# Kernel tuning notes

Hardware: AMD Instinct MI355X
Metric: run time of the kernel (lower is better)

The kernel has to match this reference:

```python
import jax, jax.numpy as jnp
import numpy as np


def setup_inputs() -> dict:
    key = jax.random.key(0)
    ks = jax.random.split(key, 16)
    B, P, N, E = 16, 12, 20000, 320000
    f32 = jnp.float32
    x = jax.random.normal(ks[0], (B, P, N), f32)
    input_mask = (jax.random.uniform(ks[1], (B, P, N)) > 0.2).astype(f32)  # GAIN observed mask
    noise = jax.random.uniform(ks[2], (B, P, N), f32) * 0.01  # Uniform(0, 0.01) noise matrix
    edge_index = jax.random.randint(ks[3], (2, E), 0, N)
    edge_weights = jax.random.uniform(ks[4], (E,), f32)

    def lin(k, fi, fo):
        return jax.random.normal(k, (fi, fo), f32) * (1.0 / np.sqrt(fi))

    params = dict(
        Wz=lin(ks[5], 2, P), bz=jnp.zeros((P,), f32),
        Wr=lin(ks[6], 2, P), br=jnp.zeros((P,), f32),
        Wh=lin(ks[7], 2, P), bh=jnp.zeros((P,), f32),
        Lz_w=lin(ks[8], 2 * P, P), Lz_b=jnp.zeros((P,), f32),
        Lr_w=lin(ks[9], 2 * P, P), Lr_b=jnp.zeros((P,), f32),
        Lh_w=lin(ks[10], 2 * P, P), Lh_b=jnp.zeros((P,), f32),
        attention=jax.random.uniform(ks[11], (P,), f32),
        W1=lin(ks[12], P, P), b1=jnp.zeros((P,), f32),
        W2=lin(ks[13], P, P), b2=jnp.zeros((P,), f32),
    )
    return dict(x=x, input_mask=input_mask, noise=noise,
                edge_index=edge_index, edge_weights=edge_weights, **params)


def reference(x, input_mask, noise, edge_index, edge_weights,
              Wz, bz, Wr, br, Wh, bh,
              Lz_w, Lz_b, Lr_w, Lr_b, Lh_w, Lh_b,
              attention, W1, b1, W2, b2):
    B, P, N = x.shape
    # GAIN: fill missing entries with small uniform noise
    x = input_mask * x + (1.0 - input_mask) * noise
    # stack([x, mask]) -> [2,B,P,N]; permute(1,3,0,2) -> [B,N,2,P]; we scan over periods
    X = jnp.transpose(jnp.stack([x, input_mask], axis=2), (1, 0, 3, 2))  # [P, B, N, 2]

    # GCNConv symmetric normalization with self-loops (fill_value = 1)
    src, dst = edge_index[0], edge_index[1]
    loop = jnp.arange(N)
    src_sl = jnp.concatenate([src, loop])
    dst_sl = jnp.concatenate([dst, loop])
    w_sl = jnp.concatenate([edge_weights, jnp.ones((N,), x.dtype)])
    deg = jnp.zeros((N,), x.dtype).at[dst_sl].add(w_sl)
    dinv = jnp.where(deg > 0, deg ** -0.5, 0.0)
    norm = dinv[src_sl] * w_sl * dinv[dst_sl]  # [E + N]

    probs = jax.nn.softmax(attention)  # attention over periods
    H0 = jnp.zeros((B, N, P), x.dtype)  # A3TGCN2 never updates H -> each period sees H = 0

    def step(acc, inp):
        Xt, p = inp  # Xt: [B, N, 2]
        # aggregate raw 2-dim features then apply the (linear) GCN weight: same math,
        # far cheaper than gathering the projected [B, E, P] messages
        msgs = Xt[:, src_sl, :] * norm[None, :, None]          # [B, E+N, 2]
        agg = jnp.zeros_like(Xt).at[:, dst_sl, :].add(msgs)    # [B, N, 2]
        xz = agg @ Wz + bz
        xr = agg @ Wr + br
        xh = agg @ Wh + bh
        Z = jax.nn.sigmoid(jnp.concatenate([xz, H0], axis=-1) @ Lz_w + Lz_b)
        R = jax.nn.sigmoid(jnp.concatenate([xr, H0], axis=-1) @ Lr_w + Lr_b)
        Ht = jnp.tanh(jnp.concatenate([xh, H0 * R], axis=-1) @ Lh_w + Lh_b)
        H = Z * H0 + (1.0 - Z) * Ht
        return acc + p * H, None

    H_accum, _ = jax.lax.scan(step, H0, (X, probs))  # [B, N, P]

    # MLP head: ReLU -> Linear -> ReLU -> Linear -> Sigmoid
    h = jax.nn.relu(H_accum)
    h = jax.nn.relu(h @ W1 + b1)
    imput = jax.nn.sigmoid(h @ W2 + b2)               # [B, N, P]
    imputation = jnp.transpose(imput, (0, 2, 1))      # [B, P, N]
    res = input_mask * x + (1.0 - input_mask) * imputation
    return res, imputation
```

## Files before the change

### kernel.cpp

```cpp
#include <hip/hip_runtime.h>

#define NN 20000
#define NE 320000
#define BB 16
#define PP 12
#define NCOL 384
#define OUT_OFF (BB*PP*NN)
#define SLICES 8
#define SCOLS 48

__device__ __forceinline__ float sigmoidf_(float v) {
    return __fdividef(1.f, 1.f + __expf(-v));
}
__device__ __forceinline__ float tanh_fast(float v) {
    v = fminf(fmaxf(v, -15.f), 15.f);
    float e = __expf(-2.f * v);
    return __fdividef(1.f - e, 1.f + e);
}

__global__ __launch_bounds__(256) void init_kernel(float* deg, int* cnt) {
    int i = blockIdx.x * 256 + threadIdx.x;
    if (i < NN) { deg[i] = 1.0f; cnt[i] = 0; }
}

__global__ __launch_bounds__(256) void degcnt_kernel(const int* __restrict__ ei,
                                                     const float* __restrict__ ew,
                                                     float* deg, int* cnt) {
    int e = blockIdx.x * 256 + threadIdx.x;
    if (e < NE) {
        int d = ei[NE + e];
        atomicAdd(&deg[d], ew[e]);
        atomicAdd(&cnt[d], 1);
    }
}

__global__ __launch_bounds__(1024) void scan_kernel(const int* __restrict__ cnt,
                                                    const float* __restrict__ deg,
                                                    int* __restrict__ rowp,
                                                    int* __restrict__ cur,
                                                    float* __restrict__ dinv) {
    __shared__ int lds[1024];
    int tid = threadIdx.x;
    int base = tid * 20;
    int local[20];
    int s = 0;
    #pragma unroll
    for (int k = 0; k < 20; ++k) {
        int i = base + k;
        int v = (i < NN) ? cnt[i] : 0;
        local[k] = s;
        s += v;
    }
    lds[tid] = s;
    __syncthreads();
    for (int off = 1; off < 1024; off <<= 1) {
        int add = (tid >= off) ? lds[tid - off] : 0;
        __syncthreads();
        lds[tid] += add;
        __syncthreads();
    }
    int pre = (tid > 0) ? lds[tid - 1] : 0;
    #pragma unroll
    for (int k = 0; k < 20; ++k) {
        int i = base + k;
        if (i < NN) {
            int ex = pre + local[k];
            rowp[i] = ex; cur[i] = ex;
            float dg = deg[i];
            dinv[i] = dg > 0.f ? 1.0f / sqrtf(dg) : 0.f;
        }
    }
    if (tid == 0) rowp[NN] = lds[1023];
}

__global__ __launch_bounds__(256) void scatter_kernel(const int* __restrict__ ei,
                                                      const float* __restrict__ ew,
                                                      const float* __restrict__ dinv,
                                                      int* cur, int2* __restrict__ epk) {
    int e = blockIdx.x * 256 + threadIdx.x;
    if (e < NE) {
        int s = ei[e];
        int d = ei[NE + e];
        int pos = atomicAdd(&cur[d], 1);
        float v = dinv[s] * ew[e] * dinv[d];
        epk[pos] = make_int2(s, __float_as_int(v));
    }
}

__global__ __launch_bounds__(256) void prep_kernel(const float* __restrict__ Wz, const float* __restrict__ bz,
                                                   const float* __restrict__ Wh, const float* __restrict__ bh,
                                                   const float* __restrict__ Lzw, const float* __restrict__ Lzb,
                                                   const float* __restrict__ Lhw, const float* __restrict__ Lhb,
                                                   const float* __restrict__ att,
                                                   const float* __restrict__ W1, const float* __restrict__ b1,
                                                   const float* __restrict__ W2, const float* __restrict__ b2,
                                                   float* __restrict__ cst) {
    int t = threadIdx.x;
    if (t < PP) {
        int p = t;
        float az0 = 0.f, az1 = 0.f, cz = 0.f, ah0 = 0.f, ah1 = 0.f, ch = 0.f;
        for (int q = 0; q < PP; ++q) {
            float lz = Lzw[q * PP + p], lh = Lhw[q * PP + p];
            az0 += Wz[q] * lz;
            az1 += Wz[PP + q] * lz;
            cz  += bz[q] * lz;
            ah0 += Wh[q] * lh;
            ah1 += Wh[PP + q] * lh;
            ch  += bh[q] * lh;
        }
        cz += Lzb[p]; ch += Lhb[p];
        cst[p] = az0; cst[12 + p] = az1; cst[24 + p] = cz;
        cst[36 + p] = ah0; cst[48 + p] = ah1; cst[60 + p] = ch;
        float m = att[0];
        for (int q = 1; q < PP; ++q) m = fmaxf(m, att[q]);
        float ssum = 0.f;
        for (int q = 0; q < PP; ++q) ssum += __expf(att[q] - m);
        cst[72 + p] = __expf(att[p] - m) / ssum;
    }
    if (t < 144) { cst[84 + t] = W1[t]; cst[240 + t] = W2[t]; }
    if (t < PP) { cst[228 + t] = b1[t]; cst[384 + t] = b2[t]; }
}

#define TILE 32
__global__ __launch_bounds__(256) void buildx_kernel(const float* __restrict__ x,
                                                     const float* __restrict__ mask,
                                                     const float* __restrict__ noise,
                                                     float* __restrict__ X) {
    __shared__ float tile[TILE][NCOL + 1];
    int tid = threadIdx.x;
    int n0 = blockIdx.x * TILE;
    int i = tid & 31;
    int prb = tid >> 5;
    #pragma unroll 4
    for (int it = 0; it < 24; ++it) {
        int pr = it * 8 + prb;
        int g = pr * NN + n0 + i;
        float m = mask[g];
        float xv = x[g];
        float nz = noise[g];
        float xf = m * xv + (1.f - m) * nz;
        int col = pr * 2;
        tile[i][col]     = xf;
        tile[i][col + 1] = m;
    }
    __syncthreads();
    #pragma unroll 4
    for (int it = 0; it < 48; ++it) {
        int idx = it * 256 + tid;
        int r = idx / NCOL;
        int c = idx - r * NCOL;
        X[(n0 + r) * NCOL + c] = tile[r][c];
    }
}

__global__ __launch_bounds__(256) void spmm_kernel(const float* __restrict__ X,
                                                   const float* __restrict__ dinv,
                                                   const int* __restrict__ rowp,
                                                   const int2* __restrict__ epk,
                                                   float* __restrict__ agg) {
    int slice = blockIdx.x & 7;
    int grp   = blockIdx.x >> 3;
    int wave = threadIdx.x >> 6;
    int lane = threadIdx.x & 63;
    int d = __builtin_amdgcn_readfirstlane(grp * 4 + wave);
    int c = slice * SCOLS + lane;
    bool act = lane < SCOLS;
    float di = dinv[d];
    float acc = 0.f;
    if (act) acc = di * di * X[(size_t)d * NCOL + c];
    int r0 = rowp[d];
    int r1 = rowp[d + 1];
    const long long* ep = (const long long*)epk;
    int e = r0;
    for (; e + 4 <= r1; e += 4) {
        long long p0 = __builtin_nontemporal_load(ep + e);
        long long p1 = __builtin_nontemporal_load(ep + e + 1);
        long long p2 = __builtin_nontemporal_load(ep + e + 2);
        long long p3 = __builtin_nontemporal_load(ep + e + 3);
        int s0 = (int)p0; float v0 = __int_as_float((int)(p0 >> 32));
        int s1 = (int)p1; float v1 = __int_as_float((int)(p1 >> 32));
        int s2 = (int)p2; float v2 = __int_as_float((int)(p2 >> 32));
        int s3 = (int)p3; float v3 = __int_as_float((int)(p3 >> 32));
        if (act) {
            float x0 = X[(size_t)s0 * NCOL + c];
            float x1 = X[(size_t)s1 * NCOL + c];
            float x2 = X[(size_t)s2 * NCOL + c];
            float x3 = X[(size_t)s3 * NCOL + c];
            acc += v0 * x0; acc += v1 * x1; acc += v2 * x2; acc += v3 * x3;
        }
    }
    for (; e < r1; ++e) {
        long long p0 = __builtin_nontemporal_load(ep + e);
        int s0 = (int)p0; float v0 = __int_as_float((int)(p0 >> 32));
        if (act) acc += v0 * X[(size_t)s0 * NCOL + c];
    }
    if (act) __builtin_nontemporal_store(acc, &agg[(size_t)d * NCOL + c]);
}

__global__ __launch_bounds__(256) void pointwise_kernel(const float* __restrict__ agg,
                                                        const float* __restrict__ cst,
                                                        const float* __restrict__ x,
                                                        const float* __restrict__ mask,
                                                        float* __restrict__ out) {
    __shared__ float C[396];
    int tid = threadIdx.x;
    for (int i = tid; i < 396; i += 256) C[i] = cst[i];
    __syncthreads();
    int idx = blockIdx.x * 256 + tid;
    int b = idx / NN;
    int n = idx - b * NN;
    float A[24];
    const float4* ap = (const float4*)(agg + (size_t)n * NCOL + b * 24);
    #pragma unroll
    for (int k = 0; k < 6; ++k) {
        float4 v = ap[k];
        A[4 * k + 0] = v.x; A[4 * k + 1] = v.y; A[4 * k + 2] = v.z; A[4 * k + 3] = v.w;
    }
    float h1[12];
    #pragma unroll
    for (int p = 0; p < 12; ++p) {
        float az0 = C[p], az1 = C[12 + p], czp = C[24 + p];
        float ah0 = C[36 + p], ah1 = C[48 + p], chp = C[60 + p];
        float hp = 0.f;
        #pragma unroll
        for (int t = 0; t < 12; ++t) {
            float a0 = A[2 * t], a1 = A[2 * t + 1];
            float z  = sigmoidf_(a0 * az0 + a1 * az1 + czp);
            float th = tanh_fast(a0 * ah0 + a1 * ah1 + chp);
            hp += C[72 + t] * ((1.f - z) * th);
        }
        h1[p] = fmaxf(hp, 0.f);
    }
    float h2[12];
    #pragma unroll
    for (int p = 0; p < 12; ++p) {
        float s = C[228 + p];
        #pragma unroll
        for (int q = 0; q < 12; ++q) s += h1[q] * C[84 + q * 12 + p];
        h2[p] = fmaxf(s, 0.f);
    }
    #pragma unroll
    for (int p = 0; p < 12; ++p) {
        float s = C[384 + p];
        #pragma unroll
        for (int q = 0; q < 12; ++q) s += h2[q] * C[240 + q * 12 + p];
        float imp = sigmoidf_(s);
        int o = (b * PP + p) * NN + n;
        float m = mask[o];
        float xv = x[o];
        out[o] = m * xv + (1.f - m) * imp;
        out[OUT_OFF + o] = imp;
    }
}

extern "C" void kernel_launch(void* const* d_in, const int* in_sizes, int n_in,
                              void* d_out, int out_size, void* d_ws, size_t ws_size,
                              hipStream_t stream) {
    const float* x     = (const float*)d_in[0];
    const float* mask  = (const float*)d_in[1];
    const float* noise = (const float*)d_in[2];
    const int*   ei    = (const int*)d_in[3];
    const float* ew    = (const float*)d_in[4];
    const float* Wz    = (const float*)d_in[5];
    const float* bz    = (const float*)d_in[6];
    const float* Wh    = (const float*)d_in[9];
    const float* bh    = (const float*)d_in[10];
    const float* Lzw   = (const float*)d_in[11];
    const float* Lzb   = (const float*)d_in[12];
    const float* Lhw   = (const float*)d_in[15];
    const float* Lhb   = (const float*)d_in[16];
    const float* att   = (const float*)d_in[17];
    const float* W1    = (const float*)d_in[18];
    const float* b1    = (const float*)d_in[19];
    const float* W2    = (const float*)d_in[20];
    const float* b2    = (const float*)d_in[21];
    float* out = (float*)d_out;

    float* Xf   = (float*)d_ws;
    float* AGG  = Xf + (size_t)NN * NCOL;
    int2*  EPK  = (int2*)(AGG + (size_t)NN * NCOL);
    float* DEG  = (float*)(EPK + NE);
    float* DINV = DEG + NN;
    float* CST  = DINV + NN;
    int*   CNT  = (int*)(CST + 512);
    int*   ROWP = CNT + NN;
    int*   CUR  = ROWP + NN + 1;

    hipLaunchKernelGGL(init_kernel,    dim3((NN + 255) / 256), dim3(256), 0, stream, DEG, CNT);
    hipLaunchKernelGGL(degcnt_kernel,  dim3((NE + 255) / 256), dim3(256), 0, stream, ei, ew, DEG, CNT);
    hipLaunchKernelGGL(scan_kernel,    dim3(1), dim3(1024), 0, stream, CNT, DEG, ROWP, CUR, DINV);
    hipLaunchKernelGGL(scatter_kernel, dim3((NE + 255) / 256), dim3(256), 0, stream, ei, ew, DINV, CUR, EPK);
    hipLaunchKernelGGL(prep_kernel,    dim3(1), dim3(256), 0, stream,
                       Wz, bz, Wh, bh, Lzw, Lzb, Lhw, Lhb, att, W1, b1, W2, b2, CST);
    hipLaunchKernelGGL(buildx_kernel,  dim3(NN / TILE), dim3(256), 0, stream, x, mask, noise, Xf);
    hipLaunchKernelGGL(spmm_kernel,    dim3(SLICES * NN / 4), dim3(256), 0, stream, Xf, DINV, ROWP, EPK, AGG);
    hipLaunchKernelGGL(pointwise_kernel, dim3((BB * NN) / 256), dim3(256), 0, stream, AGG, CST, x, mask, out);
}
```

Before: 378.8 us.

## Software-pipeline edge loads in SpMM and store aggregates in batch-major layout

The SpMM loop now prefetches the next 8 packed (src, weight) edge entries into registers while processing the current 8, and drops the nontemporal hint on those edge loads. This is meant to hide edge-list load latency behind the feature gathers. The aggregation output moves from node-major [N][384] to batch-major [B][N][24], so the pointwise kernel's per-thread float4 reads become contiguous across adjacent threads. The cost is more registers and clamped redundant loads on short rows, plus a scattered store pattern in the SpMM.

```diff
diff --git a/kernel.cpp b/kernel.cpp
--- a/kernel.cpp
+++ b/kernel.cpp
@@ -156,45 +156,54 @@
 __global__ __launch_bounds__(256) void spmm_kernel(const float* __restrict__ X,
                                                    const float* __restrict__ dinv,
                                                    const int* __restrict__ rowp,
-                                                   const int2* __restrict__ epk,
+                                                   const long long* __restrict__ ep,
                                                    float* __restrict__ agg) {
     int slice = blockIdx.x & 7;
     int grp   = blockIdx.x >> 3;
-    int wave = threadIdx.x >> 6;
-    int lane = threadIdx.x & 63;
+    int wave  = threadIdx.x >> 6;
+    int lane  = threadIdx.x & 63;
     int d = __builtin_amdgcn_readfirstlane(grp * 4 + wave);
     int c = slice * SCOLS + lane;
     bool act = lane < SCOLS;
     float di = dinv[d];
-    float acc = 0.f;
-    if (act) acc = di * di * X[(size_t)d * NCOL + c];
+    float acc = act ? di * di * X[(size_t)d * NCOL + c] : 0.f;
     int r0 = rowp[d];
     int r1 = rowp[d + 1];
-    const long long* ep = (const long long*)epk;
-    int e = r0;
-    for (; e + 4 <= r1; e += 4) {
-        long long p0 = __builtin_nontemporal_load(ep + e);
-        long long p1 = __builtin_nontemporal_load(ep + e + 1);
-        long long p2 = __builtin_nontemporal_load(ep + e + 2);
-        long long p3 = __builtin_nontemporal_load(ep + e + 3);
-        int s0 = (int)p0; float v0 = __int_as_float((int)(p0 >> 32));
-        int s1 = (int)p1; float v1 = __int_as_float((int)(p1 >> 32));
-        int s2 = (int)p2; float v2 = __int_as_float((int)(p2 >> 32));
-        int s3 = (int)p3; float v3 = __int_as_float((int)(p3 >> 32));
-        if (act) {
-            float x0 = X[(size_t)s0 * NCOL + c];
-            float x1 = X[(size_t)s1 * NCOL + c];
-            float x2 = X[(size_t)s2 * NCOL + c];
-            float x3 = X[(size_t)s3 * NCOL + c];
-            acc += v0 * x0; acc += v1 * x1; acc += v2 * x2; acc += v3 * x3;
-        }
-    }
-    for (; e < r1; ++e) {
-        long long p0 = __builtin_nontemporal_load(ep + e);
-        int s0 = (int)p0; float v0 = __int_as_float((int)(p0 >> 32));
-        if (act) acc += v0 * X[(size_t)s0 * NCOL + c];
-    }
-    if (act) __builtin_nontemporal_store(acc, &agg[(size_t)d * NCOL + c]);
+    if (r0 < r1) {
+        long long q[8], p[8];
+        int e = r0;
+        #pragma unroll
+        for (int k = 0; k < 8; ++k) {
+            int ix = e + k; ix = ix < r1 ? ix : r1 - 1;
+            q[k] = ep[ix];
+        }
+        while (e < r1) {
+            #pragma unroll
+            for (int k = 0; k < 8; ++k) p[k] = q[k];
+            int en = e + 8;
+            if (en < r1) {
+                #pragma unroll
+                for (int k = 0; k < 8; ++k) {
+                    int ix = en + k; ix = ix < r1 ? ix : r1 - 1;
+                    q[k] = ep[ix];
+                }
+            }
+            #pragma unroll
+            for (int k = 0; k < 8; ++k) {
+                if (e + k < r1) {
+                    int s = (int)p[k];
+                    float v = __int_as_float((int)(p[k] >> 32));
+                    if (act) acc += v * X[(size_t)s * NCOL + c];
+                }
+            }
+            e = en;
+        }
+    }
+    if (act) {
+        int b = slice * 2 + (lane >= 24 ? 1 : 0);
+        int j = lane - (lane >= 24 ? 24 : 0);
+        __builtin_nontemporal_store(acc, &agg[((size_t)b * NN + d) * 24 + j]);
+    }
 }
 
 __global__ __launch_bounds__(256) void pointwise_kernel(const float* __restrict__ agg,
@@ -210,7 +219,7 @@
     int b = idx / NN;
     int n = idx - b * NN;
     float A[24];
-    const float4* ap = (const float4*)(agg + (size_t)n * NCOL + b * 24);
+    const float4* ap = (const float4*)(agg + ((size_t)b * NN + n) * 24);
     #pragma unroll
     for (int k = 0; k < 6; ++k) {
         float4 v = ap[k];
@@ -278,7 +287,7 @@
 
     float* Xf   = (float*)d_ws;
     float* AGG  = Xf + (size_t)NN * NCOL;
-    int2*  EPK  = (int2*)(AGG + (size_t)NN * NCOL);
+    long long* EPK = (long long*)(AGG + (size_t)NN * NCOL);
     float* DEG  = (float*)(EPK + NE);
     float* DINV = DEG + NN;
     float* CST  = DINV + NN;
@@ -289,7 +298,7 @@
     hipLaunchKernelGGL(init_kernel,    dim3((NN + 255) / 256), dim3(256), 0, stream, DEG, CNT);
     hipLaunchKernelGGL(degcnt_kernel,  dim3((NE + 255) / 256), dim3(256), 0, stream, ei, ew, DEG, CNT);
     hipLaunchKernelGGL(scan_kernel,    dim3(1), dim3(1024), 0, stream, CNT, DEG, ROWP, CUR, DINV);
-    hipLaunchKernelGGL(scatter_kernel, dim3((NE + 255) / 256), dim3(256), 0, stream, ei, ew, DINV, CUR, EPK);
+    hipLaunchKernelGGL(scatter_kernel, dim3((NE + 255) / 256), dim3(256), 0, stream, ei, ew, DINV, CUR, (int2*)EPK);
     hipLaunchKernelGGL(prep_kernel,    dim3(1), dim3(256), 0, stream,
                        Wz, bz, Wh, bh, Lzw, Lzb, Lhw, Lhb, att, W1, b1, W2, b2, CST);
     hipLaunchKernelGGL(buildx_kernel,  dim3(NN / TILE), dim3(256), 0, stream, x, mask, noise, Xf);
```

Result: slower. 439.5 us (+16.0%).
